# Performance work log

Measured on AMD Instinct MI355X. Metric: run time of the kernel, lower is better.

The kernel has to match this reference:

```python
import jax, jax.numpy as jnp
from jax import lax
import numpy as np

DIM = 192
NH = 6
HEAD = DIM // NH
SCALE = HEAD ** -0.5
WS = (2, 7, 7)
NW = WS[0] * WS[1] * WS[2]  # 98 tokens per window
HID = 4 * DIM
EPS = 1e-5


def _rel_index():
    # static relative-position index, computed once in numpy
    cd, ch, cw = [np.arange(s) for s in WS]
    coords = np.stack(np.meshgrid(cd, ch, cw, indexing='ij')).reshape(3, -1)  # [3, NW]
    rel = coords[:, :, None] - coords[:, None, :]          # [3, NW, NW]
    rel = rel.transpose(1, 2, 0) + np.array([WS[0] - 1, WS[1] - 1, WS[2] - 1])
    rel[:, :, 0] *= (2 * WS[1] - 1) * (2 * WS[2] - 1)
    rel[:, :, 1] *= (2 * WS[2] - 1)
    return jnp.asarray(rel.sum(-1))                         # [NW, NW] int32

REL_IDX = _rel_index()


def _ln(x, g, b):
    mu = jnp.mean(x, -1, keepdims=True)
    var = jnp.mean(jnp.square(x - mu), -1, keepdims=True)
    return (x - mu) * lax.rsqrt(var + EPS) * g + b


def setup_inputs() -> dict:
    key = jax.random.key(0)
    ks = jax.random.split(key, 10)
    B, D, H, W = 2, 16, 56, 56
    N = D * H * W
    s = 0.02
    return {
        'x': jax.random.normal(ks[0], (B, N, DIM), jnp.float32),
        'norm1_g': jnp.ones((DIM,), jnp.float32),
        'norm1_b': jnp.zeros((DIM,), jnp.float32),
        'qkv_w': jax.random.normal(ks[1], (DIM, 3 * DIM), jnp.float32) * s,
        'qkv_b': jnp.zeros((3 * DIM,), jnp.float32),
        'bias_table': jax.random.normal(ks[2], ((2 * WS[0] - 1) * (2 * WS[1] - 1) * (2 * WS[2] - 1), NH), jnp.float32) * s,
        'proj_w': jax.random.normal(ks[3], (DIM, DIM), jnp.float32) * s,
        'proj_b': jnp.zeros((DIM,), jnp.float32),
        'norm2_g': jnp.ones((DIM,), jnp.float32),
        'norm2_b': jnp.zeros((DIM,), jnp.float32),
        'fc1_w': jax.random.normal(ks[4], (DIM, HID), jnp.float32) * s,
        'fc1_b': jnp.zeros((HID,), jnp.float32),
        'dw_w': jax.random.normal(ks[5], (HID, 1, 3, 3, 3), jnp.float32) * s,  # OIDHW depthwise
        'dw_b': jnp.zeros((HID,), jnp.float32),
        'fc2_w': jax.random.normal(ks[6], (HID, DIM), jnp.float32) * s,
        'fc2_b': jnp.zeros((DIM,), jnp.float32),
        'D': D, 'H': H, 'W': W,
    }


def reference(x, norm1_g, norm1_b, qkv_w, qkv_b, bias_table, proj_w, proj_b,
              norm2_g, norm2_b, fc1_w, fc1_b, dw_w, dw_b, fc2_w, fc2_b, D, H, W):
    B, N, C = x.shape
    Wd, Wh, Ww = WS
    nd, nh, nw = D // Wd, H // Wh, W // Ww

    # --- windowed attention branch ---
    h = _ln(x, norm1_g, norm1_b).reshape(B, D, H, W, C)
    h = h.reshape(B, nd, Wd, nh, Wh, nw, Ww, C)
    h = h.transpose(0, 1, 3, 5, 2, 4, 6, 7).reshape(-1, NW, C)  # [Bw, NW, C]
    Bw = h.shape[0]

    qkv = (h @ qkv_w + qkv_b).reshape(Bw, NW, 3, NH, HEAD)
    qkv = qkv.transpose(2, 0, 3, 1, 4)                           # [3, Bw, NH, NW, HEAD]
    q, k, v = qkv[0] * SCALE, qkv[1], qkv[2]

    attn = jnp.einsum('bhnd,bhmd->bhnm', q, k)                   # [Bw, NH, NW, NW]
    rel_bias = bias_table[REL_IDX]                               # [NW, NW, NH]
    attn = attn + rel_bias.transpose(2, 0, 1)[None]
    attn = jax.nn.softmax(attn, axis=-1)

    o = jnp.einsum('bhnm,bhmd->bhnd', attn, v)                   # [Bw, NH, NW, HEAD]
    o = o.transpose(0, 2, 1, 3).reshape(Bw, NW, C)
    o = o @ proj_w + proj_b

    # window reverse
    o = o.reshape(B, nd, nh, nw, Wd, Wh, Ww, C)
    o = o.transpose(0, 1, 4, 2, 5, 3, 6, 7).reshape(B, N, C)

    x = x + 0.5 * o  # DropPath scale_residual=0.5 in eval

    # --- MixFFN3D branch ---
    h = _ln(x, norm2_g, norm2_b)
    h = h @ fc1_w + fc1_b                                        # [B, N, HID]
    h = h.transpose(0, 2, 1).reshape(B, HID, D, H, W)
    h = lax.conv_general_dilated(
        h, dw_w, window_strides=(1, 1, 1), padding=[(1, 1)] * 3,
        dimension_numbers=('NCDHW', 'OIDHW', 'NCDHW'),
        feature_group_count=HID) + dw_b[None, :, None, None, None]
    h = h.reshape(B, HID, N).transpose(0, 2, 1)
    h = jax.nn.gelu(h, approximate=False)
    h = h @ fc2_w + fc2_b

    return x + 0.5 * h
```

## Files before the change

kernel.cpp:

```cpp
#include <hip/hip_runtime.h>
#include <hip/hip_bf16.h>

typedef unsigned short u16;
typedef unsigned int   u32;
typedef __bf16 bf16x8 __attribute__((ext_vector_type(8)));
typedef float  f32x4  __attribute__((ext_vector_type(4)));
typedef float  f32x2  __attribute__((ext_vector_type(2)));

#define M_TOK 100352
#define M_HALF 50176
#define DIMC  192
#define HIDC  768
#define SCALE_F 0.17677669529663688f

__device__ __forceinline__ float b2f(u16 u) {
    u32 x = ((u32)u) << 16; float f; __builtin_memcpy(&f, &x, 4); return f;
}
__device__ __forceinline__ u16 f2b(float f) {
    u32 x; __builtin_memcpy(&x, &f, 4);
    x = x + 0x7FFFu + ((x >> 16) & 1u);
    return (u16)(x >> 16);
}
__device__ __forceinline__ float lo2f(u32 w) {
    u32 x = w << 16; float f; __builtin_memcpy(&f, &x, 4); return f;
}
__device__ __forceinline__ float hi2f(u32 w) {
    u32 x = w & 0xFFFF0000u; float f; __builtin_memcpy(&f, &x, 4); return f;
}

__global__ __launch_bounds__(256) void prep_weights(
    const float* __restrict__ qkv_w, const float* __restrict__ proj_w,
    const float* __restrict__ fc1_w, const float* __restrict__ fc2_w,
    const float* __restrict__ dw_w,
    u16* __restrict__ qkvt, u16* __restrict__ projt, u16* __restrict__ fc1t,
    u16* __restrict__ fc2t, float* __restrict__ dwtf)
{
    int id = blockIdx.x * 256 + threadIdx.x;
    if (id < 110592)      { int n = id / 192, k = id % 192;                 qkvt[id] = f2b(qkv_w[k * 576 + n]); }
    else if (id < 147456) { int e = id - 110592, n = e / 192, k = e % 192;  projt[e] = f2b(proj_w[k * 192 + n]); }
    else if (id < 294912) { int e = id - 147456, n = e / 192, k = e % 192;  fc1t[e]  = f2b(fc1_w[k * 768 + n]); }
    else if (id < 442368) { int e = id - 294912, n = e / 768, k = e % 768;  fc2t[e]  = f2b(fc2_w[k * 192 + n]); }
    else if (id < 463104) { int e = id - 442368, t = e / 768, c = e % 768;  dwtf[e]  = dw_w[c * 27 + t]; }
}

__global__ __launch_bounds__(256) void biasmat_kernel(
    const float* __restrict__ btab, float* __restrict__ bmat)
{
    int id = blockIdx.x * 256 + threadIdx.x;
    if (id >= 6 * 112 * 112) return;
    int h = id / 12544, rem = id % 12544, i = rem / 112, j = rem % 112;
    float v;
    if (j >= 98)      v = -1e30f;
    else if (i >= 98) v = 0.0f;
    else {
        int di = i / 49, hi = (i / 7) % 7, wi = i % 7;
        int dj = j / 49, hj = (j / 7) % 7, wj = j % 7;
        int idx = (di - dj + 1) * 169 + (hi - hj + 6) * 13 + (wi - wj + 6);
        v = btab[idx * 6 + h];
    }
    bmat[id] = v;
}

template<bool PERM, bool BF_IN>
__global__ __launch_bounds__(256) void ln_kernel(
    const void* __restrict__ xin, const float* __restrict__ g,
    const float* __restrict__ bb, u16* __restrict__ out)
{
    int row  = blockIdx.x * 4 + (threadIdx.x >> 6);
    int lane = threadIdx.x & 63;
    float v0, v1, v2;
    if (BF_IN) {
        const u16* xr = (const u16*)xin + (size_t)row * DIMC;
        v0 = b2f(xr[lane]); v1 = b2f(xr[lane + 64]); v2 = b2f(xr[lane + 128]);
    } else {
        const float* xr = (const float*)xin + (size_t)row * DIMC;
        v0 = xr[lane]; v1 = xr[lane + 64]; v2 = xr[lane + 128];
    }
    float s  = v0 + v1 + v2;
    float s2 = v0 * v0 + v1 * v1 + v2 * v2;
    #pragma unroll
    for (int m = 1; m < 64; m <<= 1) { s += __shfl_xor(s, m); s2 += __shfl_xor(s2, m); }
    float mu = s * (1.0f / 192.0f);
    float rs = rsqrtf(s2 * (1.0f / 192.0f) - mu * mu + 1e-5f);
    size_t ob;
    if (PERM) {
        int b = row / 50176, r = row % 50176;
        int d = r / 3136, r2 = r % 3136, h = r2 / 56, w = r2 % 56;
        int widx = ((b * 8 + (d >> 1)) * 8 + h / 7) * 8 + w / 7;
        int tok  = (d & 1) * 49 + (h % 7) * 7 + (w % 7);
        ob = ((size_t)widx * 98 + tok) * DIMC;
    } else {
        ob = (size_t)row * DIMC;
    }
    out[ob + lane]       = f2b((v0 - mu) * rs * g[lane]       + bb[lane]);
    out[ob + lane + 64]  = f2b((v1 - mu) * rs * g[lane + 64]  + bb[lane + 64]);
    out[ob + lane + 128] = f2b((v2 - mu) * rs * g[lane + 128] + bb[lane + 128]);
}

template<int EPI>
__global__ __launch_bounds__(256) void gemm_bt(
    const u16* __restrict__ A, const u16* __restrict__ Bt,
    const float* __restrict__ bias, int K, int N,
    u16* __restrict__ outb, const float* __restrict__ xres,
    u16* __restrict__ x2b, float* __restrict__ outf, int mofs)
{
    __shared__ __align__(16) u16 Alds[128 * 32];
    __shared__ __align__(16) u16 Blds[64 * 32];
    int m0 = blockIdx.x * 128;
    int n0 = blockIdx.y * 64;
    int t  = threadIdx.x;
    int ar = t >> 2, ac = (t & 3) * 8;
    int lane = t & 63, wid = t >> 6;
    int wm = wid >> 1, wn = wid & 1;
    int lrow = lane & 15, lko = (lane >> 4) * 8;
    const u16* Ab  = A  + (size_t)(m0 + ar) * K + ac;
    const u16* Ab2 = Ab + (size_t)64 * K;
    const u16* Bb  = Bt + (size_t)(n0 + ar) * K + ac;
    f32x4 acc[4][2] = {};
    for (int kt = 0; kt < K; kt += 32) {
        uint4 a0 = *(const uint4*)(Ab  + kt);
        uint4 a1 = *(const uint4*)(Ab2 + kt);
        uint4 b0 = *(const uint4*)(Bb  + kt);
        __syncthreads();
        ((uint4*)Alds)[t]       = a0;
        ((uint4*)Alds)[256 + t] = a1;
        ((uint4*)Blds)[t]       = b0;
        __syncthreads();
        bf16x8 af[4], bfr[2];
        #pragma unroll
        for (int mi = 0; mi < 4; mi++)
            af[mi] = *(const bf16x8*)&Alds[(wm * 64 + mi * 16 + lrow) * 32 + lko];
        #pragma unroll
        for (int ni = 0; ni < 2; ni++)
            bfr[ni] = *(const bf16x8*)&Blds[(wn * 32 + ni * 16 + lrow) * 32 + lko];
        #pragma unroll
        for (int mi = 0; mi < 4; mi++)
            #pragma unroll
            for (int ni = 0; ni < 2; ni++)
                acc[mi][ni] = __builtin_amdgcn_mfma_f32_16x16x32_bf16(af[mi], bfr[ni], acc[mi][ni], 0, 0, 0);
    }
    int r0 = (lane >> 4) * 4, cl = lane & 15;
    #pragma unroll
    for (int ni = 0; ni < 2; ni++) {
        int col = n0 + wn * 32 + ni * 16 + cl;
        float bv = bias[col];
        #pragma unroll
        for (int mi = 0; mi < 4; mi++) {
            #pragma unroll
            for (int r = 0; r < 4; r++) {
                int row = m0 + wm * 64 + mi * 16 + r0 + r;
                float v = acc[mi][ni][r] + bv;
                if (EPI == 0) {
                    outb[(size_t)row * N + col] = f2b(v);
                } else if (EPI == 1) {
                    int widx = row / 98, tok = row % 98;
                    int b = widx >> 9, rem = widx & 511;
                    int bd = rem >> 6, bh = (rem >> 3) & 7, bw = rem & 7;
                    int td = tok / 49, rr = tok % 49, th = rr / 7, tw = rr % 7;
                    int d = bd * 2 + td, h = bh * 7 + th, w = bw * 7 + tw;
                    size_t gg = ((size_t)b * 50176 + (d * 56 + h) * 56 + w) * (size_t)N + col;
                    x2b[gg] = f2b(xres[gg] + 0.5f * v);
                } else {
                    size_t gg = (size_t)(row + mofs) * N + col;
                    outf[gg] = b2f(x2b[gg]) + 0.5f * v;
                }
            }
        }
    }
}

__global__ __launch_bounds__(64) void attn_mfma_kernel(
    const u16* __restrict__ qkv, const float* __restrict__ bmat,
    u16* __restrict__ outb)
{
    __shared__ __align__(16) u16 Klds[112 * 40];
    __shared__ __align__(16) u16 Vt[32 * 136];
    __shared__ __align__(16) u16 Plds[16 * 136];
    int widx = blockIdx.x, head = blockIdx.y;
    int l = threadIdx.x;
    int c = l & 15, g = l >> 4;
    size_t wbase = (size_t)widx * (98 * 576) + head * 32;

    for (int e = l; e < 448; e += 64) {
        int rr = e >> 2, seg = (e & 3) * 8;
        uint4 kr = {0, 0, 0, 0}, vr = {0, 0, 0, 0};
        if (rr < 98) {
            kr = *(const uint4*)(qkv + wbase + (size_t)rr * 576 + 192 + seg);
            vr = *(const uint4*)(qkv + wbase + (size_t)rr * 576 + 384 + seg);
        }
        *(uint4*)&Klds[rr * 40 + seg] = kr;
        int sw = ((seg >> 3) & 3) << 4;
        int pc = rr ^ sw;
        const u16* vp = (const u16*)&vr;
        #pragma unroll
        for (int u = 0; u < 8; u++)
            Vt[(seg + u) * 136 + pc] = vp[u];
    }
    {
        int d = l >> 1, half = l & 1;
        int sw = ((d >> 3) & 3) << 4;
        uint4 z = {0, 0, 0, 0};
        *(uint4*)&Vt[d * 136 + ((112 + 8 * half) ^ sw)] = z;
        if (l < 32) {
            int i = l >> 1; half = l & 1;
            int swp = ((i >> 2) & 3) << 4;
            *(uint4*)&Plds[i * 136 + ((112 + 8 * half) ^ swp)] = z;
        }
    }

    for (int it = 0; it < 7; ++it) {
        int qtok = 16 * it + c; if (qtok > 97) qtok = 97;
        bf16x8 qf = *(const bf16x8*)(qkv + wbase + (size_t)qtok * 576 + g * 8);
        f32x4 s[7];
        f32x4 z = {};
        #pragma unroll
        for (int jt = 0; jt < 7; ++jt) {
            bf16x8 kf = *(const bf16x8*)&Klds[(16 * jt + c) * 40 + g * 8];
            s[jt] = __builtin_amdgcn_mfma_f32_16x16x32_bf16(qf, kf, z, 0, 0, 0);
        }
        const float* bb = bmat + ((size_t)head * 112 + 16 * it + 4 * g) * 112 + c;
        float sm[4];
        #pragma unroll
        for (int r = 0; r < 4; ++r) {
            float m = -1e30f;
            #pragma unroll
            for (int jt = 0; jt < 7; ++jt) {
                float v = s[jt][r] * SCALE_F + bb[r * 112 + 16 * jt];
                s[jt][r] = v;
                m = fmaxf(m, v);
            }
            m = fmaxf(m, __shfl_xor(m, 1)); m = fmaxf(m, __shfl_xor(m, 2));
            m = fmaxf(m, __shfl_xor(m, 4)); m = fmaxf(m, __shfl_xor(m, 8));
            float su = 0.f;
            #pragma unroll
            for (int jt = 0; jt < 7; ++jt) {
                float p = __expf(s[jt][r] - m);
                s[jt][r] = p;
                su += p;
            }
            su += __shfl_xor(su, 1); su += __shfl_xor(su, 2);
            su += __shfl_xor(su, 4); su += __shfl_xor(su, 8);
            sm[r] = su;
        }
        #pragma unroll
        for (int r = 0; r < 4; ++r) {
            int prow = 4 * g + r;
            int swp = ((prow >> 2) & 3) << 4;
            #pragma unroll
            for (int jt = 0; jt < 7; ++jt)
                Plds[prow * 136 + ((16 * jt + c) ^ swp)] = f2b(s[jt][r]);
        }
        bf16x8 pa[4];
        int swr = ((c >> 2) & 3) << 4;
        #pragma unroll
        for (int ks = 0; ks < 4; ++ks)
            pa[ks] = *(const bf16x8*)&Plds[c * 136 + ((32 * ks + 8 * g) ^ swr)];
        #pragma unroll
        for (int dt = 0; dt < 2; ++dt) {
            f32x4 o = {};
            int vrow = 16 * dt + c;
            int swv = ((vrow >> 3) & 3) << 4;
            #pragma unroll
            for (int ks = 0; ks < 4; ++ks) {
                bf16x8 vb = *(const bf16x8*)&Vt[vrow * 136 + ((32 * ks + 8 * g) ^ swv)];
                o = __builtin_amdgcn_mfma_f32_16x16x32_bf16(pa[ks], vb, o, 0, 0, 0);
            }
            #pragma unroll
            for (int r = 0; r < 4; ++r) {
                int row = 16 * it + 4 * g + r;
                if (row < 98)
                    outb[((size_t)widx * 98 + row) * DIMC + head * 32 + 16 * dt + c]
                        = f2b(o[r] / sm[r]);
            }
        }
    }
}

__global__ __launch_bounds__(256, 8) void dwconv_gelu_kernel(
    const u16* __restrict__ hid, const float* __restrict__ dwtf,
    const float* __restrict__ dwb, u16* __restrict__ outb)
{
    int gid = blockIdx.x * 256 + threadIdx.x;
    int cg = gid % 96;
    int t  = gid / 96;
    int d  = t & 15;
    t >>= 4;
    int wg = t % 28;
    int h  = t / 28;
    int w0 = wg * 2;
    int c0 = cg * 8;

    f32x2 acc[2][4];
    {
        float4 b0 = *(const float4*)(dwb + c0);
        float4 b1 = *(const float4*)(dwb + c0 + 4);
        #pragma unroll
        for (int wi = 0; wi < 2; ++wi) {
            acc[wi][0] = f32x2{b0.x, b0.y};
            acc[wi][1] = f32x2{b0.z, b0.w};
            acc[wi][2] = f32x2{b1.x, b1.y};
            acc[wi][3] = f32x2{b1.z, b1.w};
        }
    }

    #pragma unroll
    for (int iz = 0; iz < 3; ++iz) {
        int zz = d - 1 + iz;
        if ((unsigned)zz >= 16u) continue;
        #pragma unroll
        for (int iy = 0; iy < 3; ++iy) {
            int yy = h - 1 + iy;
            if ((unsigned)yy >= 56u) continue;
            uint4 raw[4];
            const u16* rp = hid + ((size_t)(zz * 56 + yy) * 56 + w0 - 1) * HIDC + c0;
            #pragma unroll
            for (int ix = 0; ix < 4; ++ix) {
                uint4 iv = {0, 0, 0, 0};
                if ((unsigned)(w0 - 1 + ix) < 56u)
                    iv = *(const uint4*)(rp + (size_t)ix * HIDC);
                raw[ix] = iv;
            }
            const float* wrow = dwtf + (size_t)(iz * 9 + iy * 3) * HIDC + c0;
            #pragma unroll
            for (int hf = 0; hf < 2; ++hf) {
                f32x2 inf[4][2];
                #pragma unroll
                for (int p = 0; p < 4; ++p) {
                    u32 wa = hf ? raw[p].z : raw[p].x;
                    u32 wb = hf ? raw[p].w : raw[p].y;
                    inf[p][0] = f32x2{lo2f(wa), hi2f(wa)};
                    inf[p][1] = f32x2{lo2f(wb), hi2f(wb)};
                }
                #pragma unroll
                for (int dx = 0; dx < 3; ++dx) {
                    float4 wv = *(const float4*)(wrow + dx * HIDC + hf * 4);
                    f32x2 wp0 = f32x2{wv.x, wv.y};
                    f32x2 wp1 = f32x2{wv.z, wv.w};
                    acc[0][hf * 2 + 0] += inf[dx][0] * wp0;
                    acc[0][hf * 2 + 1] += inf[dx][1] * wp1;
                    acc[1][hf * 2 + 0] += inf[dx + 1][0] * wp0;
                    acc[1][hf * 2 + 1] += inf[dx + 1][1] * wp1;
                }
            }
        }
    }

    size_t tok0 = (size_t)(d * 56 + h) * 56 + w0;
    #pragma unroll
    for (int wi = 0; wi < 2; ++wi) {
        u16 res[8];
        #pragma unroll
        for (int pr = 0; pr < 4; ++pr) {
            #pragma unroll
            for (int u = 0; u < 2; ++u) {
                float a = acc[wi][pr][u];
                float tt = a * (1.5957691216f + 0.0713548162f * a * a);
                float n = __expf(-tt);
                res[pr * 2 + u] = f2b(a / (1.0f + n));
            }
        }
        uint4 ov;
        u32* op = (u32*)&ov;
        op[0] = (u32)res[0] | ((u32)res[1] << 16);
        op[1] = (u32)res[2] | ((u32)res[3] << 16);
        op[2] = (u32)res[4] | ((u32)res[5] << 16);
        op[3] = (u32)res[6] | ((u32)res[7] << 16);
        *(uint4*)(outb + (tok0 + wi) * HIDC + c0) = ov;
    }
}

extern "C" void kernel_launch(void* const* d_in, const int* in_sizes, int n_in,
                              void* d_out, int out_size, void* d_ws, size_t ws_size,
                              hipStream_t stream)
{
    const float* x      = (const float*)d_in[0];
    const float* n1g    = (const float*)d_in[1];
    const float* n1b    = (const float*)d_in[2];
    const float* qkv_w  = (const float*)d_in[3];
    const float* qkv_b  = (const float*)d_in[4];
    const float* btab   = (const float*)d_in[5];
    const float* proj_w = (const float*)d_in[6];
    const float* proj_b = (const float*)d_in[7];
    const float* n2g    = (const float*)d_in[8];
    const float* n2b    = (const float*)d_in[9];
    const float* fc1_w  = (const float*)d_in[10];
    const float* fc1_b  = (const float*)d_in[11];
    const float* dw_w   = (const float*)d_in[12];
    const float* dw_b   = (const float*)d_in[13];
    const float* fc2_w  = (const float*)d_in[14];
    const float* fc2_b  = (const float*)d_in[15];

    char* ws = (char*)d_ws;
    u16*   qkvt  = (u16*)(ws);
    u16*   projt = (u16*)(ws + 221184);
    u16*   fc1t  = (u16*)(ws + 294912);
    u16*   fc2t  = (u16*)(ws + 589824);
    float* dwtf  = (float*)(ws + 884736);
    u16*   r1    = (u16*)(ws + 1160192);
    u16*   qkvb  = (u16*)(ws + 39695360LL);
    u16*   x2b   = (u16*)(ws + 39695360LL);
    u16*   hid_c = (u16*)(ws + 78230528LL);
    float* bmat  = (float*)(ws + 155300864LL);
    u16*   gelu_c= (u16*)(ws + 155300864LL);

    prep_weights<<<dim3(1809), dim3(256), 0, stream>>>(qkv_w, proj_w, fc1_w, fc2_w, dw_w,
                                                       qkvt, projt, fc1t, fc2t, dwtf);
    biasmat_kernel<<<dim3(294), dim3(256), 0, stream>>>(btab, bmat);
    ln_kernel<true, false><<<dim3(25088), dim3(256), 0, stream>>>(x, n1g, n1b, r1);
    gemm_bt<0><<<dim3(784, 9), dim3(256), 0, stream>>>(r1, qkvt, qkv_b, 192, 576,
                                                       qkvb, nullptr, nullptr, nullptr, 0);
    attn_mfma_kernel<<<dim3(1024, 6), dim3(64), 0, stream>>>(qkvb, bmat, r1);
    gemm_bt<1><<<dim3(784, 3), dim3(256), 0, stream>>>(r1, projt, proj_b, 192, 192,
                                                       nullptr, x, x2b, nullptr, 0);
    ln_kernel<false, true><<<dim3(25088), dim3(256), 0, stream>>>(x2b, n2g, n2b, r1);
    for (int b = 0; b < 2; b++) {
        const u16* h2c = r1 + (size_t)b * M_HALF * DIMC;
        gemm_bt<0><<<dim3(392, 12), dim3(256), 0, stream>>>(h2c, fc1t, fc1_b, 192, 768,
                                                            hid_c, nullptr, nullptr, nullptr, 0);
        dwconv_gelu_kernel<<<dim3(9408), dim3(256), 0, stream>>>(hid_c, dwtf, dw_b, gelu_c);
        gemm_bt<2><<<dim3(392, 3), dim3(256), 0, stream>>>(gelu_c, fc2t, fc2_b, 768, 192,
                                                           nullptr, nullptr, x2b, (float*)d_out,
                                                           b * M_HALF);
    }
}
```

Baseline: 837.8 us.

## Use direct global-to-LDS loads, XCD-aware block swizzle, and retile depthwise conv

The GEMM now fills its shared-memory tiles with global_load_lds, skipping the trip through registers, and runs on a 1D grid. Block IDs are remapped with an 8-way swizzle so that consecutive tiles land on the same XCD and can share L2. The depthwise conv+GELU kernel now gives each thread 4 channels by 4 consecutive W positions instead of 8 channels by 2, so it loads 6 inputs per row instead of 4 and reuses each input across more outputs. The direct-to-LDS loads are issued without explicit waits beyond __syncthreads, and the narrower 8-byte conv loads may coalesce less well.

Result: faster. 728.9 us (-13.0%).

```diff
diff --git a/kernel.cpp b/kernel.cpp
--- a/kernel.cpp
+++ b/kernel.cpp
@@ -26,6 +26,11 @@
 }
 __device__ __forceinline__ float hi2f(u32 w) {
     u32 x = w & 0xFFFF0000u; float f; __builtin_memcpy(&f, &x, 4); return f;
+}
+__device__ __forceinline__ void g2l16(const u16* g, u16* l) {
+    __builtin_amdgcn_global_load_lds(
+        (const __attribute__((address_space(1))) u32*)g,
+        (__attribute__((address_space(3))) u32*)l, 16, 0, 0);
 }
 
 __global__ __launch_bounds__(256) void prep_weights(
@@ -100,31 +105,34 @@
 template<int EPI>
 __global__ __launch_bounds__(256) void gemm_bt(
     const u16* __restrict__ A, const u16* __restrict__ Bt,
-    const float* __restrict__ bias, int K, int N,
+    const float* __restrict__ bias, int K, int N, int NBN,
     u16* __restrict__ outb, const float* __restrict__ xres,
     u16* __restrict__ x2b, float* __restrict__ outf, int mofs)
 {
     __shared__ __align__(16) u16 Alds[128 * 32];
     __shared__ __align__(16) u16 Blds[64 * 32];
-    int m0 = blockIdx.x * 128;
-    int n0 = blockIdx.y * 64;
+    int bid = blockIdx.x;
+    int cpx = gridDim.x >> 3;
+    int swz = (bid & 7) * cpx + (bid >> 3);
+    int m0 = (swz / NBN) * 128;
+    int n0 = (swz % NBN) * 64;
     int t  = threadIdx.x;
     int ar = t >> 2, ac = (t & 3) * 8;
     int lane = t & 63, wid = t >> 6;
     int wm = wid >> 1, wn = wid & 1;
     int lrow = lane & 15, lko = (lane >> 4) * 8;
-    const u16* Ab  = A  + (size_t)(m0 + ar) * K + ac;
-    const u16* Ab2 = Ab + (size_t)64 * K;
-    const u16* Bb  = Bt + (size_t)(n0 + ar) * K + ac;
+    const u16* Ag  = A  + (size_t)(m0 + ar) * K + ac;
+    const u16* Ag2 = Ag + (size_t)64 * K;
+    const u16* Bg  = Bt + (size_t)(n0 + ar) * K + ac;
+    u16* lA  = Alds + t * 8;
+    u16* lA2 = Alds + 2048 + t * 8;
+    u16* lB  = Blds + t * 8;
     f32x4 acc[4][2] = {};
     for (int kt = 0; kt < K; kt += 32) {
-        uint4 a0 = *(const uint4*)(Ab  + kt);
-        uint4 a1 = *(const uint4*)(Ab2 + kt);
-        uint4 b0 = *(const uint4*)(Bb  + kt);
         __syncthreads();
-        ((uint4*)Alds)[t]       = a0;
-        ((uint4*)Alds)[256 + t] = a1;
-        ((uint4*)Blds)[t]       = b0;
+        g2l16(Ag  + kt, lA);
+        g2l16(Ag2 + kt, lA2);
+        g2l16(Bg  + kt, lB);
         __syncthreads();
         bf16x8 af[4], bfr[2];
         #pragma unroll
@@ -280,26 +288,25 @@
     const u16* __restrict__ hid, const float* __restrict__ dwtf,
     const float* __restrict__ dwb, u16* __restrict__ outb)
 {
-    int gid = blockIdx.x * 256 + threadIdx.x;
-    int cg = gid % 96;
-    int t  = gid / 96;
+    int bid = blockIdx.x;
+    int swz = (bid & 7) * 1176 + (bid >> 3);
+    int gid = swz * 256 + threadIdx.x;
+    int cg = gid % 192;
+    int t  = gid / 192;
     int d  = t & 15;
     t >>= 4;
-    int wg = t % 28;
-    int h  = t / 28;
-    int w0 = wg * 2;
-    int c0 = cg * 8;
-
-    f32x2 acc[2][4];
+    int wg = t % 14;
+    int h  = t / 14;
+    int w0 = wg * 4;
+    int c0 = cg * 4;
+
+    f32x2 acc[4][2];
     {
-        float4 b0 = *(const float4*)(dwb + c0);
-        float4 b1 = *(const float4*)(dwb + c0 + 4);
-        #pragma unroll
-        for (int wi = 0; wi < 2; ++wi) {
-            acc[wi][0] = f32x2{b0.x, b0.y};
-            acc[wi][1] = f32x2{b0.z, b0.w};
-            acc[wi][2] = f32x2{b1.x, b1.y};
-            acc[wi][3] = f32x2{b1.z, b1.w};
+        float4 bv = *(const float4*)(dwb + c0);
+        #pragma unroll
+        for (int wi = 0; wi < 4; ++wi) {
+            acc[wi][0] = f32x2{bv.x, bv.y};
+            acc[wi][1] = f32x2{bv.z, bv.w};
         }
     }
 
@@ -311,35 +318,32 @@
         for (int iy = 0; iy < 3; ++iy) {
             int yy = h - 1 + iy;
             if ((unsigned)yy >= 56u) continue;
-            uint4 raw[4];
+            uint2 raw[6];
             const u16* rp = hid + ((size_t)(zz * 56 + yy) * 56 + w0 - 1) * HIDC + c0;
             #pragma unroll
-            for (int ix = 0; ix < 4; ++ix) {
-                uint4 iv = {0, 0, 0, 0};
+            for (int ix = 0; ix < 6; ++ix) {
+                uint2 iv = {0, 0};
                 if ((unsigned)(w0 - 1 + ix) < 56u)
-                    iv = *(const uint4*)(rp + (size_t)ix * HIDC);
+                    iv = *(const uint2*)(rp + (size_t)ix * HIDC);
                 raw[ix] = iv;
             }
             const float* wrow = dwtf + (size_t)(iz * 9 + iy * 3) * HIDC + c0;
-            #pragma unroll
-            for (int hf = 0; hf < 2; ++hf) {
-                f32x2 inf[4][2];
-                #pragma unroll
-                for (int p = 0; p < 4; ++p) {
-                    u32 wa = hf ? raw[p].z : raw[p].x;
-                    u32 wb = hf ? raw[p].w : raw[p].y;
-                    inf[p][0] = f32x2{lo2f(wa), hi2f(wa)};
-                    inf[p][1] = f32x2{lo2f(wb), hi2f(wb)};
-                }
+            float4 wv0 = *(const float4*)(wrow);
+            float4 wv1 = *(const float4*)(wrow + HIDC);
+            float4 wv2 = *(const float4*)(wrow + 2 * HIDC);
+            f32x2 wp[3][2] = {
+                { f32x2{wv0.x, wv0.y}, f32x2{wv0.z, wv0.w} },
+                { f32x2{wv1.x, wv1.y}, f32x2{wv1.z, wv1.w} },
+                { f32x2{wv2.x, wv2.y}, f32x2{wv2.z, wv2.w} } };
+            #pragma unroll
+            for (int p = 0; p < 6; ++p) {
+                f32x2 i0 = f32x2{lo2f(raw[p].x), hi2f(raw[p].x)};
+                f32x2 i1 = f32x2{lo2f(raw[p].y), hi2f(raw[p].y)};
                 #pragma unroll
                 for (int dx = 0; dx < 3; ++dx) {
-                    float4 wv = *(const float4*)(wrow + dx * HIDC + hf * 4);
-                    f32x2 wp0 = f32x2{wv.x, wv.y};
-                    f32x2 wp1 = f32x2{wv.z, wv.w};
-                    acc[0][hf * 2 + 0] += inf[dx][0] * wp0;
-                    acc[0][hf * 2 + 1] += inf[dx][1] * wp1;
-                    acc[1][hf * 2 + 0] += inf[dx + 1][0] * wp0;
-                    acc[1][hf * 2 + 1] += inf[dx + 1][1] * wp1;
+                    if (dx > p || dx < p - 3) continue;
+                    acc[p - dx][0] += i0 * wp[dx][0];
+                    acc[p - dx][1] += i1 * wp[dx][1];
                 }
             }
         }
@@ -347,25 +351,21 @@
 
     size_t tok0 = (size_t)(d * 56 + h) * 56 + w0;
     #pragma unroll
-    for (int wi = 0; wi < 2; ++wi) {
-        u16 res[8];
-        #pragma unroll
-        for (int pr = 0; pr < 4; ++pr) {
+    for (int wi = 0; wi < 4; ++wi) {
+        u16 res[4];
+        #pragma unroll
+        for (int pr = 0; pr < 2; ++pr) {
             #pragma unroll
             for (int u = 0; u < 2; ++u) {
                 float a = acc[wi][pr][u];
                 float tt = a * (1.5957691216f + 0.0713548162f * a * a);
-                float n = __expf(-tt);
-                res[pr * 2 + u] = f2b(a / (1.0f + n));
-            }
-        }
-        uint4 ov;
-        u32* op = (u32*)&ov;
-        op[0] = (u32)res[0] | ((u32)res[1] << 16);
-        op[1] = (u32)res[2] | ((u32)res[3] << 16);
-        op[2] = (u32)res[4] | ((u32)res[5] << 16);
-        op[3] = (u32)res[6] | ((u32)res[7] << 16);
-        *(uint4*)(outb + (tok0 + wi) * HIDC + c0) = ov;
+                res[pr * 2 + u] = f2b(a / (1.0f + __expf(-tt)));
+            }
+        }
+        uint2 ov;
+        ov.x = (u32)res[0] | ((u32)res[1] << 16);
+        ov.y = (u32)res[2] | ((u32)res[3] << 16);
+        *(uint2*)(outb + (tok0 + wi) * HIDC + c0) = ov;
     }
 }
 
@@ -407,19 +407,19 @@
                                                        qkvt, projt, fc1t, fc2t, dwtf);
     biasmat_kernel<<<dim3(294), dim3(256), 0, stream>>>(btab, bmat);
     ln_kernel<true, false><<<dim3(25088), dim3(256), 0, stream>>>(x, n1g, n1b, r1);
-    gemm_bt<0><<<dim3(784, 9), dim3(256), 0, stream>>>(r1, qkvt, qkv_b, 192, 576,
-                                                       qkvb, nullptr, nullptr, nullptr, 0);
+    gemm_bt<0><<<dim3(7056), dim3(256), 0, stream>>>(r1, qkvt, qkv_b, 192, 576, 9,
+                                                     qkvb, nullptr, nullptr, nullptr, 0);
     attn_mfma_kernel<<<dim3(1024, 6), dim3(64), 0, stream>>>(qkvb, bmat, r1);
-    gemm_bt<1><<<dim3(784, 3), dim3(256), 0, stream>>>(r1, projt, proj_b, 192, 192,
-                                                       nullptr, x, x2b, nullptr, 0);
+    gemm_bt<1><<<dim3(2352), dim3(256), 0, stream>>>(r1, projt, proj_b, 192, 192, 3,
+                                                     nullptr, x, x2b, nullptr, 0);
     ln_kernel<false, true><<<dim3(25088), dim3(256), 0, stream>>>(x2b, n2g, n2b, r1);
     for (int b = 0; b < 2; b++) {
         const u16* h2c = r1 + (size_t)b * M_HALF * DIMC;
-        gemm_bt<0><<<dim3(392, 12), dim3(256), 0, stream>>>(h2c, fc1t, fc1_b, 192, 768,
-                                                            hid_c, nullptr, nullptr, nullptr, 0);
+        gemm_bt<0><<<dim3(4704), dim3(256), 0, stream>>>(h2c, fc1t, fc1_b, 192, 768, 12,
+                                                         hid_c, nullptr, nullptr, nullptr, 0);
         dwconv_gelu_kernel<<<dim3(9408), dim3(256), 0, stream>>>(hid_c, dwtf, dw_b, gelu_c);
-        gemm_bt<2><<<dim3(392, 3), dim3(256), 0, stream>>>(gelu_c, fc2t, fc2_b, 768, 192,
-                                                           nullptr, nullptr, x2b, (float*)d_out,
-                                                           b * M_HALF);
-    }
-}
+        gemm_bt<2><<<dim3(1176), dim3(256), 0, stream>>>(gelu_c, fc2t, fc2_b, 768, 192, 3,
+                                                         nullptr, nullptr, x2b, (float*)d_out,
+                                                         b * M_HALF);
+    }
+}
```
